# Kernel tuning notes

Measured on AMD Instinct MI355X. Metric: run time of the kernel, lower is better.

## Reference

```python
import jax, jax.numpy as jnp
import numpy as np

N_JOINTS = 16
N_VERTS = 778
# standard MANO kinematic tree (parent of joint i; root parent is -1, unused)
PARENTS = np.array([-1, 0, 1, 2, 0, 4, 5, 0, 7, 8, 0, 10, 11, 0, 13, 14])
# rotate_base=True: root rotation is post-multiplied by 180-deg rotation about x
ROT_X = np.array([[1.0, 0.0, 0.0], [0.0, -1.0, 0.0], [0.0, 0.0, -1.0]], dtype=np.float32)


def _batch_rodrigues(theta):
    # theta: [M, 3] axis-angle -> [M, 3, 3] rotation matrices (via quaternion, HMR-style)
    angle = jnp.linalg.norm(theta + 1e-8, axis=1, keepdims=True)
    axis = theta / angle
    half = 0.5 * angle
    quat = jnp.concatenate([jnp.cos(half), jnp.sin(half) * axis], axis=1)
    quat = quat / jnp.linalg.norm(quat, axis=1, keepdims=True)
    w, x, y, z = quat[:, 0], quat[:, 1], quat[:, 2], quat[:, 3]
    w2, x2, y2, z2 = w * w, x * x, y * y, z * z
    wx, wy, wz = w * x, w * y, w * z
    xy, xz, yz = x * y, x * z, y * z
    R = jnp.stack([
        w2 + x2 - y2 - z2, 2 * xy - 2 * wz, 2 * wy + 2 * xz,
        2 * wz + 2 * xy, w2 - x2 + y2 - z2, 2 * yz - 2 * wx,
        2 * xz - 2 * wy, 2 * wx + 2 * yz, w2 - x2 - y2 + z2,
    ], axis=1)
    return R.reshape(-1, 3, 3)


def _make_A(R, t):
    # R: [N,3,3], t: [N,3] -> [N,4,4] homogeneous transform
    top = jnp.concatenate([R, t[:, :, None]], axis=2)          # [N,3,4]
    bot = jnp.broadcast_to(jnp.array([0.0, 0.0, 0.0, 1.0], R.dtype), (R.shape[0], 1, 4))
    return jnp.concatenate([top, bot], axis=1)


def _global_rigid_transform(Rs, J):
    # Rs: [N,16,3,3], J: [N,16,3]
    root_rotation = jnp.matmul(Rs[:, 0], jnp.asarray(ROT_X, Rs.dtype))
    results = [_make_A(root_rotation, J[:, 0])]
    for i in range(1, N_JOINTS):
        p = int(PARENTS[i])
        t = J[:, i] - J[:, p]
        results.append(jnp.matmul(results[p], _make_A(Rs[:, i], t)))
    G = jnp.stack(results, axis=1)                              # [N,16,4,4]
    J_transformed = G[:, :, :3, 3]
    # A = G - pad(G[:, :, :3, :3] @ J) : remove joint-rest translation
    rel = jnp.einsum('njab,njb->nja', G[:, :, :3, :3], J)       # [N,16,3]
    A = G.at[:, :, :3, 3].add(-rel)
    return J_transformed, A


def setup_inputs() -> dict:
    key = jax.random.key(0)
    ks = jax.random.split(key, 7)
    N = 4096
    return {
        'beta': jax.random.normal(ks[0], (N, 10), jnp.float32),
        'theta': jax.random.normal(ks[1], (N, 48), jnp.float32) * 0.3,
        'v_template': jax.random.normal(ks[2], (N_VERTS, 3), jnp.float32) * 0.1,
        'shapedirs': jax.random.normal(ks[3], (10, N_VERTS * 3), jnp.float32) * 0.01,
        'J_regressor': jax.random.uniform(ks[4], (N_VERTS, N_JOINTS), jnp.float32) / N_VERTS,
        'posedirs': jax.random.normal(ks[5], (135, N_VERTS * 3), jnp.float32) * 0.01,
        'weights': jax.random.uniform(ks[6], (N_VERTS, N_JOINTS), jnp.float32),
    }


def reference(beta, theta, v_template, shapedirs, J_regressor, posedirs, weights):
    N = beta.shape[0]
    # shape blendshapes
    v_shaped = jnp.matmul(beta, shapedirs).reshape(N, N_VERTS, 3) + v_template
    # rest joints from vertices
    J = jnp.einsum('nvc,vj->njc', v_shaped, J_regressor)        # [N,16,3]
    # pose rotations
    Rs = _batch_rodrigues(theta.reshape(-1, 3)).reshape(N, N_JOINTS, 3, 3)
    # pose blendshapes (exclude root)
    pose_feature = (Rs[:, 1:] - jnp.eye(3, dtype=Rs.dtype)).reshape(N, 135)
    v_posed = jnp.matmul(pose_feature, posedirs).reshape(N, N_VERTS, 3) + v_shaped
    # kinematic chain
    J_transformed, A = _global_rigid_transform(Rs, J)
    # linear blend skinning
    T = jnp.einsum('vj,njab->nvab', weights, A)                 # [N,778,4,4]
    ones = jnp.ones((N, N_VERTS, 1), v_posed.dtype)
    v_homo = jnp.concatenate([v_posed, ones], axis=2)           # [N,778,4]
    verts = jnp.einsum('nvab,nvb->nva', T, v_homo)[:, :, :3]    # [N,778,3]
    joints = jnp.einsum('nvc,vj->njc', verts, J_regressor)      # [N,16,3]
    return verts, joints, Rs
```

## Files before the change

kernel.cpp:

```cpp
#include <hip/hip_runtime.h>
#include <math.h>

#define NJ 16
#define NV 778
#define M3 2334
#define NTB 156

typedef float f32x4  __attribute__((ext_vector_type(4)));
typedef short bf16x8 __attribute__((ext_vector_type(8)));

__device__ __forceinline__ unsigned short f2bf(float x) {
    unsigned int u = __float_as_uint(x);
    unsigned int r = (u + 0x7FFF + ((u >> 16) & 1)) >> 16;
    return (unsigned short)r;
}

__device__ __forceinline__ void rodrigues9(
    float t0, float t1, float t2,
    float& r0, float& r1, float& r2, float& r3, float& r4,
    float& r5, float& r6, float& r7, float& r8)
{
    const float eps = 1e-8f;
    float a0 = t0 + eps, a1 = t1 + eps, a2 = t2 + eps;
    float angle = sqrtf(a0*a0 + a1*a1 + a2*a2);
    float inv  = 1.0f / angle;
    float half = 0.5f * angle;
    float sh = sinf(half), chh = cosf(half);
    float qw = chh;
    float qx = sh * t0 * inv;
    float qy = sh * t1 * inv;
    float qz = sh * t2 * inv;
    float qn = 1.0f / sqrtf(qw*qw + qx*qx + qy*qy + qz*qz);
    qw *= qn; qx *= qn; qy *= qn; qz *= qn;
    float w2=qw*qw, x2=qx*qx, y2=qy*qy, z2=qz*qz;
    float wx=qw*qx, wy=qw*qy, wz=qw*qz;
    float xy=qx*qy, xz=qx*qz, yz=qy*qz;
    r0 = w2 + x2 - y2 - z2;
    r1 = 2.f*(xy - wz);
    r2 = 2.f*(wy + xz);
    r3 = 2.f*(wz + xy);
    r4 = w2 - x2 + y2 - z2;
    r5 = 2.f*(yz - wx);
    r6 = 2.f*(xz - wy);
    r7 = 2.f*(wx + yz);
    r8 = w2 - x2 - y2 + z2;
}


__global__ __launch_bounds__(256, 1) void k01_prep(
    const float* __restrict__ shapedirs,
    const float* __restrict__ posedirs,
    const float* __restrict__ Jreg,
    const float* __restrict__ vtemp,
    const float* __restrict__ theta,
    const float* __restrict__ beta,
    float* __restrict__ SJJT,
    float* __restrict__ RsOut,
    bf16x8* __restrict__ Bf,
    bf16x8* __restrict__ Af,
    int N)
{
    const int tid = threadIdx.x;
    const int rodBlocks = (N * NJ) / 256;
    const int nB = NTB * 5 * 64;
    const int bfBlocks = nB / 256;
    if (blockIdx.x < 44) {
        int task = blockIdx.x * 4 + (tid >> 6);
        int lane = tid & 63;
        if (task < 176) {
            int b = task >> 4;
            int j = task & 15;
            const float* src = (b < 10) ? (shapedirs + (size_t)b * M3) : vtemp;
            float a0 = 0.f, a1 = 0.f, a2 = 0.f;
            for (int v = lane; v < NV; v += 64) {
                float jr = Jreg[v * 16 + j];
                a0 = fmaf(src[v*3 + 0], jr, a0);
                a1 = fmaf(src[v*3 + 1], jr, a1);
                a2 = fmaf(src[v*3 + 2], jr, a2);
            }
#pragma unroll
            for (int m = 1; m < 64; m <<= 1) {
                a0 += __shfl_xor(a0, m);
                a1 += __shfl_xor(a1, m);
                a2 += __shfl_xor(a2, m);
            }
            if (lane == 0) {
                int base = (b < 10) ? (b*48 + j*3) : (480 + j*3);
                SJJT[base + 0] = a0;
                SJJT[base + 1] = a1;
                SJJT[base + 2] = a2;
            }
        }
        return;
    }
    if (blockIdx.x < 44 + rodBlocks) {
        int idx = (blockIdx.x - 44) * 256 + tid;
        int n = idx >> 4;
        int j = idx & 15;
        float r0,r1,r2,r3,r4,r5,r6,r7,r8;
        rodrigues9(theta[n*48 + j*3 + 0], theta[n*48 + j*3 + 1],
                   theta[n*48 + j*3 + 2], r0,r1,r2,r3,r4,r5,r6,r7,r8);
        float* R = RsOut + (size_t)idx * 9;
        R[0]=r0; R[1]=r1; R[2]=r2; R[3]=r3; R[4]=r4;
        R[5]=r5; R[6]=r6; R[7]=r7; R[8]=r8;
        return;
    }
    if (blockIdx.x < 44 + rodBlocks + bfBlocks) {
        int idx = (blockIdx.x - 44 - rodBlocks) * 256 + tid;
        int lane = idx & 63;
        int ks   = (idx >> 6) % 5;
        int nt   = idx / 320;
        int col = nt * 16 + (lane & 15);
        int k0  = ks * 32 + (lane >> 4) * 8;
        bf16x8 o;
#pragma unroll
        for (int j = 0; j < 8; ++j) {
            int k = k0 + j;
            float val = 0.f;
            if (col < M3) {
                if (k < 10)       val = shapedirs[(size_t)k * M3 + col];
                else if (k < 145) val = posedirs[(size_t)(k - 10) * M3 + col];
            }
            o[j] = (short)f2bf(val);
        }
        Bf[idx] = o;
        return;
    }
    int idx = (blockIdx.x - 44 - rodBlocks - bfBlocks) * 256 + tid;
    int nA = (N / 16) * 5 * 64;
    if (idx >= nA) return;
    int lane = idx & 63;
    int ks   = (idx >> 6) % 5;
    int mt   = idx / 320;
    int n  = mt * 16 + (lane & 15);
    int k0 = ks * 32 + (lane >> 4) * 8;

    int kkA = k0 - 10;
    int jA  = (kkA < 0) ? 0 : (kkA > 134 ? 14 : kkA / 9);
    int kkB = k0 - 3;
    int jB  = (kkB < 0) ? 0 : (kkB > 134 ? 14 : kkB / 9);

    float ra0,ra1,ra2,ra3,ra4,ra5,ra6,ra7,ra8;
    rodrigues9(theta[n*48 + (jA+1)*3 + 0], theta[n*48 + (jA+1)*3 + 1],
               theta[n*48 + (jA+1)*3 + 2], ra0,ra1,ra2,ra3,ra4,ra5,ra6,ra7,ra8);
    float rb0,rb1,rb2,rb3,rb4,rb5,rb6,rb7,rb8;
    rodrigues9(theta[n*48 + (jB+1)*3 + 0], theta[n*48 + (jB+1)*3 + 1],
               theta[n*48 + (jB+1)*3 + 2], rb0,rb1,rb2,rb3,rb4,rb5,rb6,rb7,rb8);

    bf16x8 o;
#pragma unroll
    for (int j = 0; j < 8; ++j) {
        int k = k0 + j;
        float val;
        if (k < 10) {
            val = beta[(size_t)n * 10 + k];
        } else if (k < 145) {
            int kk = k - 10;
            int jj = kk / 9;
            int rr = kk - jj * 9;
            float sa = (rr==0)?ra0:(rr==1)?ra1:(rr==2)?ra2:(rr==3)?ra3:
                       (rr==4)?ra4:(rr==5)?ra5:(rr==6)?ra6:(rr==7)?ra7:ra8;
            float sb = (rr==0)?rb0:(rr==1)?rb1:(rr==2)?rb2:(rr==3)?rb3:
                       (rr==4)?rb4:(rr==5)?rb5:(rr==6)?rb6:(rr==7)?rb7:rb8;
            float vv = (jj == jA) ? sa : sb;
            if ((rr & 3) == 0) vv -= 1.f;
            val = vv;
        } else {
            val = 0.f;
        }
        o[j] = (short)f2bf(val);
    }
    Af[idx] = o;
}

__global__ __launch_bounds__(256, 1) void k2c_chain(
    const float* __restrict__ beta,
    const float* __restrict__ Rs,
    const float* __restrict__ SJJT,
    float* __restrict__ Aws,
    int N)
{
    __shared__ float sS[528];
    const int tid = threadIdx.x;
    for (int i = tid; i < 528; i += 256) sS[i] = SJJT[i];
    __syncthreads();
    int gid = blockIdx.x * 256 + tid;
    if (gid >= N * 5) return;
    int n  = gid / 5;
    int ch = gid % 5;

    float b[10];
#pragma unroll
    for (int i = 0; i < 10; ++i) b[i] = beta[n*10 + i];

    int jidx[4];
    jidx[0] = 0; jidx[1] = ch*3 + 1; jidx[2] = ch*3 + 2; jidx[3] = ch*3 + 3;
    float J[4][3];
#pragma unroll
    for (int q = 0; q < 4; ++q) {
        int j = jidx[q];
#pragma unroll
        for (int c = 0; c < 3; ++c) {
            float acc = sS[480 + j*3 + c];
#pragma unroll
            for (int qq = 0; qq < 10; ++qq)
                acc = fmaf(b[qq], sS[qq*48 + j*3 + c], acc);
            J[q][c] = acc;
        }
    }

    const float* Rn = Rs + (size_t)n * 144;
    float* An = Aws + (size_t)n * 192;

    float GpR[9], Gpt[3];
#pragma unroll
    for (int r = 0; r < 3; ++r) {
        GpR[r*3+0] =  Rn[r*3+0];
        GpR[r*3+1] = -Rn[r*3+1];
        GpR[r*3+2] = -Rn[r*3+2];
    }
    Gpt[0] = J[0][0]; Gpt[1] = J[0][1]; Gpt[2] = J[0][2];

    if (ch == 0) {
#pragma unroll
        for (int r = 0; r < 3; ++r) {
            float rel = GpR[r*3+0]*J[0][0] + GpR[r*3+1]*J[0][1] + GpR[r*3+2]*J[0][2];
            An[r*4 + 0] = GpR[r*3+0];
            An[r*4 + 1] = GpR[r*3+1];
            An[r*4 + 2] = GpR[r*3+2];
            An[r*4 + 3] = Gpt[r] - rel;
        }
    }

#pragma unroll
    for (int st = 0; st < 3; ++st) {
        int i = jidx[st+1];
        const float* Ri = Rn + (size_t)i * 9;
        float t0 = J[st+1][0] - J[st][0];
        float t1 = J[st+1][1] - J[st][1];
        float t2 = J[st+1][2] - J[st][2];
        float GR[9], Gt[3];
#pragma unroll
        for (int r = 0; r < 3; ++r) {
#pragma unroll
            for (int c = 0; c < 3; ++c)
                GR[r*3+c] = GpR[r*3+0]*Ri[c] + GpR[r*3+1]*Ri[3+c] + GpR[r*3+2]*Ri[6+c];
            Gt[r] = GpR[r*3+0]*t0 + GpR[r*3+1]*t1 + GpR[r*3+2]*t2 + Gpt[r];
        }
#pragma unroll
        for (int r = 0; r < 3; ++r) {
            float rel = GR[r*3+0]*J[st+1][0] + GR[r*3+1]*J[st+1][1] + GR[r*3+2]*J[st+1][2];
            An[i*12 + r*4 + 0] = GR[r*3+0];
            An[i*12 + r*4 + 1] = GR[r*3+1];
            An[i*12 + r*4 + 2] = GR[r*3+2];
            An[i*12 + r*4 + 3] = Gt[r] - rel;
        }
#pragma unroll
        for (int r = 0; r < 9; ++r) GpR[r] = GR[r];
        Gpt[0] = Gt[0]; Gpt[1] = Gt[1]; Gpt[2] = Gt[2];
    }
}

__global__ __launch_bounds__(256, 1) void k34_gemm_blend(
    const bf16x8* __restrict__ Af,
    const bf16x8* __restrict__ Bf,
    const float* __restrict__ vtemp,
    const float* __restrict__ Aws,
    const float* __restrict__ weights,
    float* __restrict__ verts,
    int N)
{
    __shared__ float sC[16][194];
    const int tid  = threadIdx.x;
    const int w    = tid >> 6;
    const int lane = tid & 63;
    const int mt   = blockIdx.x;
    const int ntb  = blockIdx.y * 12 + w * 3;

    f32x4 acc0 = {0.f,0.f,0.f,0.f};
    f32x4 acc1 = {0.f,0.f,0.f,0.f};
    f32x4 acc2 = {0.f,0.f,0.f,0.f};

    const bf16x8* Ab = Af + (size_t)mt * 5 * 64 + lane;
    const bf16x8* Bb = Bf + lane;

#pragma unroll
    for (int ks = 0; ks < 5; ++ks) {
        bf16x8 a  = Ab[ks * 64];
        bf16x8 b0 = Bb[((size_t)(ntb+0) * 5 + ks) * 64];
        bf16x8 b1 = Bb[((size_t)(ntb+1) * 5 + ks) * 64];
        bf16x8 b2 = Bb[((size_t)(ntb+2) * 5 + ks) * 64];
        acc0 = __builtin_amdgcn_mfma_f32_16x16x32_bf16(a, b0, acc0, 0, 0, 0);
        acc1 = __builtin_amdgcn_mfma_f32_16x16x32_bf16(a, b1, acc1, 0, 0, 0);
        acc2 = __builtin_amdgcn_mfma_f32_16x16x32_bf16(a, b2, acc2, 0, 0, 0);
    }

    {
        const int rl = (lane >> 4) * 4;
        const int cl = w * 48 + (lane & 15);
#pragma unroll
        for (int r = 0; r < 4; ++r) {
            sC[rl + r][cl +  0] = acc0[r];
            sC[rl + r][cl + 16] = acc1[r];
            sC[rl + r][cl + 32] = acc2[r];
        }
    }
    __syncthreads();

    const int vg = blockIdx.y * 64 + lane;
    const bool valid = vg < NV;
    const int cvg = valid ? vg : (NV - 1);

    const float4* wrow = reinterpret_cast<const float4*>(&weights[(size_t)cvg * 16]);
    float vtx = vtemp[cvg*3 + 0];
    float vty = vtemp[cvg*3 + 1];
    float vtz = vtemp[cvg*3 + 2];

#pragma unroll
    for (int it = 0; it < 4; ++it) {
        const int nl = w * 4 + it;
        const int n  = __builtin_amdgcn_readfirstlane(mt * 16 + nl);
        const float* An = Aws + (size_t)n * 192;

        float px = sC[nl][lane*3 + 0] + vtx;
        float py = sC[nl][lane*3 + 1] + vty;
        float pz = sC[nl][lane*3 + 2] + vtz;

        float ox = 0.f, oy = 0.f, oz = 0.f;
#pragma unroll
        for (int q = 0; q < 4; ++q) {
            float4 wq = wrow[q];
#define BJQ(jj_, ww_) { \
            const float* ap = An + (4*q + jj_) * 12; \
            float a0=ap[0], a1=ap[1], a2 =ap[2],  a3 =ap[3]; \
            float a4=ap[4], a5=ap[5], a6 =ap[6],  a7 =ap[7]; \
            float a8=ap[8], a9=ap[9], a10=ap[10], a11=ap[11]; \
            float X = fmaf(a0,px, fmaf(a1,py, fmaf(a2,pz, a3))); \
            float Y = fmaf(a4,px, fmaf(a5,py, fmaf(a6,pz, a7))); \
            float Z = fmaf(a8,px, fmaf(a9,py, fmaf(a10,pz, a11))); \
            ox = fmaf(ww_, X, ox); oy = fmaf(ww_, Y, oy); oz = fmaf(ww_, Z, oz); }
            BJQ(0, wq.x) BJQ(1, wq.y) BJQ(2, wq.z) BJQ(3, wq.w)
#undef BJQ
        }

        if (valid) {
            float* o = verts + (size_t)(mt*16 + nl) * M3 + (size_t)vg * 3;
            o[0] = ox; o[1] = oy; o[2] = oz;
        }
    }
}

__global__ __launch_bounds__(256, 1) void k4b_joints(
    const float* __restrict__ verts,
    const float* __restrict__ Jreg,
    float* __restrict__ joints,
    int N)
{
    __shared__ float part[4][4][48];
    const int tid = threadIdx.x;
    const int nl  = tid >> 6;
    const int sub = tid & 63;
    const int j   = sub & 15;
    const int c4  = sub >> 4;
    const int n   = blockIdx.x * 4 + nl;

    int vbeg = c4 * 195;
    int vend = vbeg + 195; if (vend > NV) vend = NV;

    const float* vp = verts + (size_t)n * M3;
    float a0 = 0.f, a1 = 0.f, a2 = 0.f;
#pragma unroll 4
    for (int v = vbeg; v < vend; ++v) {
        float jr = Jreg[(size_t)v * 16 + j];
        float x = vp[v*3 + 0], y = vp[v*3 + 1], z = vp[v*3 + 2];
        a0 = fmaf(jr, x, a0);
        a1 = fmaf(jr, y, a1);
        a2 = fmaf(jr, z, a2);
    }
    part[nl][c4][j*3+0] = a0;
    part[nl][c4][j*3+1] = a1;
    part[nl][c4][j*3+2] = a2;
    __syncthreads();

    if (tid < 192) {
        int nl2 = tid / 48;
        int r   = tid % 48;
        float s = part[nl2][0][r] + part[nl2][1][r] + part[nl2][2][r] + part[nl2][3][r];
        joints[(size_t)(blockIdx.x * 4 + nl2) * 48 + r] = s;
    }
}

extern "C" void kernel_launch(void* const* d_in, const int* in_sizes, int n_in,
                              void* d_out, int out_size, void* d_ws, size_t ws_size,
                              hipStream_t stream)
{
    const float* beta   = (const float*)d_in[0];
    const float* theta  = (const float*)d_in[1];
    const float* vtemp  = (const float*)d_in[2];
    const float* shaped = (const float*)d_in[3];
    const float* Jreg   = (const float*)d_in[4];
    const float* posed  = (const float*)d_in[5];
    const float* wts    = (const float*)d_in[6];
    float* out = (float*)d_out;
    const int N = in_sizes[0] / 10;

    float* verts  = out;
    float* joints = out + (size_t)N * M3;
    float* RsOut  = joints + (size_t)N * 48;
    float* Aws    = (float*)d_ws;
    float*  fbase = Aws + (size_t)N * 192;
    bf16x8* Af    = (bf16x8*)fbase;
    bf16x8* Bf    = (bf16x8*)(fbase + (size_t)(N/16)*5*64*4);

    const int nA = (N / 16) * 5 * 64;
    const int nB = NTB * 5 * 64;
    const int rodBlocks = (N * NJ) / 256;

    k01_prep<<<44 + rodBlocks + nB/256 + nA/256, 256, 0, stream>>>(
        shaped, posed, Jreg, vtemp, theta, beta, joints, RsOut, Bf, Af, N);
    k2c_chain<<<(N*5 + 255)/256, 256, 0, stream>>>(beta, RsOut, joints, Aws, N);
    k34_gemm_blend<<<dim3(N/16, 13), 256, 0, stream>>>(
        Af, Bf, vtemp, Aws, wts, verts, N);
    k4b_joints<<<N/4, 256, 0, stream>>>(verts, Jreg, joints, N);
}
```

Baseline: 83.84 us.

## Fuse joint regression into blend kernel using shared-memory verts and atomics

```diff
diff --git a/kernel.cpp b/kernel.cpp
--- a/kernel.cpp
+++ b/kernel.cpp
@@ -178,10 +178,17 @@
     const float* __restrict__ Rs,
     const float* __restrict__ SJJT,
     float* __restrict__ Aws,
+    float* __restrict__ joints,
     int N)
 {
+    const int tid = threadIdx.x;
+    const int KB = (N * 5 + 255) / 256;
+    if (blockIdx.x >= KB) {
+        int idx = (blockIdx.x - KB) * 256 + tid;
+        if (idx < N * 48) joints[idx] = 0.f;
+        return;
+    }
     __shared__ float sS[528];
-    const int tid = threadIdx.x;
     for (int i = tid; i < 528; i += 256) sS[i] = SJJT[i];
     __syncthreads();
     int gid = blockIdx.x * 256 + tid;
@@ -267,7 +274,9 @@
     const float* __restrict__ vtemp,
     const float* __restrict__ Aws,
     const float* __restrict__ weights,
+    const float* __restrict__ Jreg,
     float* __restrict__ verts,
+    float* __restrict__ joints,
     int N)
 {
     __shared__ float sC[16][194];
@@ -316,6 +325,7 @@
     float vty = vtemp[cvg*3 + 1];
     float vtz = vtemp[cvg*3 + 2];
 
+    float res[12];
 #pragma unroll
     for (int it = 0; it < 4; ++it) {
         const int nl = w * 4 + it;
@@ -342,51 +352,39 @@
             BJQ(0, wq.x) BJQ(1, wq.y) BJQ(2, wq.z) BJQ(3, wq.w)
 #undef BJQ
         }
-
+        res[it*3+0] = ox; res[it*3+1] = oy; res[it*3+2] = oz;
+    }
+    __syncthreads();
+
+#pragma unroll
+    for (int it = 0; it < 4; ++it) {
+        const int nl = w * 4 + it;
+        sC[nl][lane*3 + 0] = res[it*3+0];
+        sC[nl][lane*3 + 1] = res[it*3+1];
+        sC[nl][lane*3 + 2] = res[it*3+2];
         if (valid) {
             float* o = verts + (size_t)(mt*16 + nl) * M3 + (size_t)vg * 3;
-            o[0] = ox; o[1] = oy; o[2] = oz;
-        }
-    }
-}
-
-__global__ __launch_bounds__(256, 1) void k4b_joints(
-    const float* __restrict__ verts,
-    const float* __restrict__ Jreg,
-    float* __restrict__ joints,
-    int N)
-{
-    __shared__ float part[4][4][48];
-    const int tid = threadIdx.x;
-    const int nl  = tid >> 6;
-    const int sub = tid & 63;
-    const int j   = sub & 15;
-    const int c4  = sub >> 4;
-    const int n   = blockIdx.x * 4 + nl;
-
-    int vbeg = c4 * 195;
-    int vend = vbeg + 195; if (vend > NV) vend = NV;
-
-    const float* vp = verts + (size_t)n * M3;
-    float a0 = 0.f, a1 = 0.f, a2 = 0.f;
+            o[0] = res[it*3+0]; o[1] = res[it*3+1]; o[2] = res[it*3+2];
+        }
+    }
+    __syncthreads();
+
+    {
+        const int s  = tid >> 4;
+        const int j  = tid & 15;
+        const int vb = blockIdx.y * 64;
+        float a0 = 0.f, a1 = 0.f, a2 = 0.f;
 #pragma unroll 4
-    for (int v = vbeg; v < vend; ++v) {
-        float jr = Jreg[(size_t)v * 16 + j];
-        float x = vp[v*3 + 0], y = vp[v*3 + 1], z = vp[v*3 + 2];
-        a0 = fmaf(jr, x, a0);
-        a1 = fmaf(jr, y, a1);
-        a2 = fmaf(jr, z, a2);
-    }
-    part[nl][c4][j*3+0] = a0;
-    part[nl][c4][j*3+1] = a1;
-    part[nl][c4][j*3+2] = a2;
-    __syncthreads();
-
-    if (tid < 192) {
-        int nl2 = tid / 48;
-        int r   = tid % 48;
-        float s = part[nl2][0][r] + part[nl2][1][r] + part[nl2][2][r] + part[nl2][3][r];
-        joints[(size_t)(blockIdx.x * 4 + nl2) * 48 + r] = s;
+        for (int v = 0; v < 64; ++v) {
+            float jr = (vb + v < NV) ? Jreg[(size_t)(vb + v) * 16 + j] : 0.f;
+            a0 = fmaf(jr, sC[s][v*3 + 0], a0);
+            a1 = fmaf(jr, sC[s][v*3 + 1], a1);
+            a2 = fmaf(jr, sC[s][v*3 + 2], a2);
+        }
+        float* jp = joints + (size_t)(mt * 16 + s) * 48 + j * 3;
+        atomicAdd(&jp[0], a0);
+        atomicAdd(&jp[1], a1);
+        atomicAdd(&jp[2], a2);
     }
 }
 
@@ -409,17 +407,19 @@
     float* RsOut  = joints + (size_t)N * 48;
     float* Aws    = (float*)d_ws;
     float*  fbase = Aws + (size_t)N * 192;
-    bf16x8* Af    = (bf16x8*)fbase;
-    bf16x8* Bf    = (bf16x8*)(fbase + (size_t)(N/16)*5*64*4);
-
     const int nA = (N / 16) * 5 * 64;
     const int nB = NTB * 5 * 64;
+    bf16x8* Af    = (bf16x8*)fbase;
+    bf16x8* Bf    = (bf16x8*)(fbase + (size_t)nA * 4);
+    float*  sjjt  = fbase + (size_t)nA * 4 + (size_t)nB * 4;
+
     const int rodBlocks = (N * NJ) / 256;
+    const int zeroBlocks = (N * 48 + 255) / 256;
 
     k01_prep<<<44 + rodBlocks + nB/256 + nA/256, 256, 0, stream>>>(
-        shaped, posed, Jreg, vtemp, theta, beta, joints, RsOut, Bf, Af, N);
-    k2c_chain<<<(N*5 + 255)/256, 256, 0, stream>>>(beta, RsOut, joints, Aws, N);
+        shaped, posed, Jreg, vtemp, theta, beta, sjjt, RsOut, Bf, Af, N);
+    k2c_chain<<<(N*5 + 255)/256 + zeroBlocks, 256, 0, stream>>>(
+        beta, RsOut, sjjt, Aws, joints, N);
     k34_gemm_blend<<<dim3(N/16, 13), 256, 0, stream>>>(
-        Af, Bf, vtemp, Aws, wts, verts, N);
-    k4b_joints<<<N/4, 256, 0, stream>>>(verts, Jreg, joints, N);
-}
+        Af, Bf, vtemp, Aws, wts, Jreg, verts, joints, N);
+}
```

New measurement: 69.77 us, median of 2. 16.8% less time.
